# Performance work log

Hardware: AMD Instinct MI355X
Metric: run time of the kernel (lower is better)

## Reference

```python
import jax, jax.numpy as jnp
import numpy as np

B, T, D_IN, H, D = 4, 4096, 1024, 16, 64


def setup_inputs() -> dict:
    key = jax.random.key(0)
    k1, k2, k3 = jax.random.split(key, 3)
    inputs = jax.random.normal(k1, (B, T, D_IN), dtype=jnp.float32)
    kv_kernel = jax.random.normal(k2, (D_IN, H, D, 2), dtype=jnp.float32) * (1.0 / np.sqrt(D_IN))
    q_kernel = jax.random.normal(k3, (H, D), dtype=jnp.float32) * (1.0 / np.sqrt(D))
    return {"inputs": inputs, "kv_kernel": kv_kernel, "q_kernel": q_kernel}


def _associate(a, b):
    # Online-softmax combine on packed tuples [m(1), u(1), w(D)] along last axis.
    ma, ua, wa = a[..., :1], a[..., 1:2], a[..., 2:]
    mb, ub, wb = b[..., :1], b[..., 1:2], b[..., 2:]
    m = jnp.maximum(ma, mb)
    ea = jnp.exp(ma - m)
    eb = jnp.exp(mb - m)
    u = ua * ea + ub * eb
    w = wa * ea + wb * eb
    return jnp.concatenate([m, u, w], axis=-1)


def reference(inputs, kv_kernel, q_kernel):
    # inputs: (B,T,D_in); kv_kernel: (D_in,H,D,2); q_kernel: (H,D)
    kv = jnp.einsum('bti,ihdk->bthdk', inputs, kv_kernel)
    kv = jax.nn.relu(kv)  # activation; dropout disabled (inference)
    k = kv[..., 0]  # (B,T,H,D)
    v = kv[..., 1]  # (B,T,H,D)
    st = jnp.einsum('hd,bthd->bth', q_kernel, k)[..., None]  # (B,T,H,1)
    u_init = jnp.ones_like(st)  # exp(s - m) with m = s
    elems = jnp.concatenate([st, u_init, v], axis=-1)  # (B,T,H,D+2)
    o = jax.lax.associative_scan(_associate, elems, axis=1)
    c = o[..., 1:2]  # running denominator
    a = o[..., 2:]   # running numerator (B,T,H,D)
    h = a / c
    # concat_heads=False -> sum over heads
    return jnp.sum(h, axis=-2)  # (B,T,D)
```

## Files before the change

### kernel.cpp

```cpp
#include <hip/hip_runtime.h>
#include <hip/hip_bf16.h>
#include <math.h>

#define B_   4
#define T_   4096
#define DIN_ 1024
#define H_   16
#define D_   64
#define M_   (B_*T_)
#define N_   (H_*D_*2)
#define K_   DIN_
#define C_   64
#define CL_  (T_/C_)

typedef unsigned short u16;
typedef __attribute__((ext_vector_type(8))) short short8_t;
typedef __attribute__((ext_vector_type(4))) float float4_t;

__device__ __forceinline__ u16 f2bf(float f) {
  unsigned int x = __float_as_uint(f);
  x += 0x7fffu + ((x >> 16) & 1u);
  return (u16)(x >> 16);
}
__device__ __forceinline__ float bf2f(unsigned int u) {
  return __uint_as_float((u & 0xffffu) << 16);
}

__device__ __forceinline__ void g2l16(const u16* g, u16* l) {
  __builtin_amdgcn_global_load_lds(
      (const __attribute__((address_space(1))) void*)g,
      (__attribute__((address_space(3))) void*)l, 16, 0, 0);
}

__global__ __launch_bounds__(256)
void prep(const float* __restrict__ inputs, const float* __restrict__ kvk,
          u16* __restrict__ aB, u16* __restrict__ wBt) {
  __shared__ float tile[32][33];
  int bid = blockIdx.x;
  int tid = threadIdx.x;
  if (bid < 8192) {
    int i = bid * 256 + tid;
    const float4* src = (const float4*)inputs;
    float4 a = src[2*i], b = src[2*i+1];
    uint4 o;
    o.x = (unsigned)f2bf(a.x) | ((unsigned)f2bf(a.y) << 16);
    o.y = (unsigned)f2bf(a.z) | ((unsigned)f2bf(a.w) << 16);
    o.z = (unsigned)f2bf(b.x) | ((unsigned)f2bf(b.y) << 16);
    o.w = (unsigned)f2bf(b.z) | ((unsigned)f2bf(b.w) << 16);
    ((uint4*)aB)[i] = o;
  } else {
    int b2 = bid - 8192;
    int kb = (b2 & 31) * 32;
    int nb = (b2 >> 5) * 32;
    int r  = tid >> 3;
    int c4 = (tid & 7) * 4;
    float4 v = *(const float4*)&kvk[(size_t)(kb + r) * N_ + nb + c4];
    tile[r][c4+0] = v.x; tile[r][c4+1] = v.y; tile[r][c4+2] = v.z; tile[r][c4+3] = v.w;
    __syncthreads();
    unsigned lo = (unsigned)f2bf(tile[c4+0][r]) | ((unsigned)f2bf(tile[c4+1][r]) << 16);
    unsigned hi = (unsigned)f2bf(tile[c4+2][r]) | ((unsigned)f2bf(tile[c4+3][r]) << 16);
    uint2 o; o.x = lo; o.y = hi;
    *(uint2*)&wBt[(size_t)(nb + r) * K_ + kb + c4] = o;
  }
}

__global__ __launch_bounds__(256)
void gemm_kv(const u16* __restrict__ A, const u16* __restrict__ Bt,
             const float* __restrict__ q,
             float* __restrict__ sbuf, u16* __restrict__ vbuf) {
  __shared__ __align__(16) char smem[27136];
  u16*   lA    = (u16*)smem;
  u16*   lB    = (u16*)(smem + 8192);
  u16*   vtile = (u16*)smem;
  float* sred  = (float*)(smem + 18432);
  __shared__ float qs[D_];

  const int tid  = threadIdx.x;
  const int wave = tid >> 6;
  const int lane = tid & 63;
  const int quad = lane >> 4;
  const int l16  = lane & 15;
  const int h    = blockIdx.x;
  const int mt   = blockIdx.y;
  const int bm = mt * 128;
  const int bn = h * 128;
  const int wm = (wave >> 1) * 64;
  const int wn = (wave & 1) * 64;

  if (tid < D_) qs[tid] = q[h * D_ + tid];

  const int r4 = lane >> 2;
  const int cc = lane & 3;
  const int gk = ((cc ^ ((r4 >> 1) & 3))) * 8;
  const u16* ga0 = A  + (size_t)(bm + wave*16 + r4) * K_ + gk;
  const u16* ga1 = ga0 + (size_t)64 * K_;
  const u16* gb0 = Bt + (size_t)(bn + wave*16 + r4) * K_ + gk;
  const u16* gb1 = gb0 + (size_t)64 * K_;
  u16* la0 = lA + (wave*16) * 32;
  u16* la1 = lA + (64 + wave*16) * 32;
  u16* lb0 = lB + (wave*16) * 32;
  u16* lb1 = lB + (64 + wave*16) * 32;

  const int swz = (quad ^ ((l16 >> 1) & 3)) * 8;

  float4_t acc[4][4] = {};

  for (int k0 = 0; k0 < K_; k0 += 32) {
    __syncthreads();
    g2l16(ga0 + k0, la0);
    g2l16(ga1 + k0, la1);
    g2l16(gb0 + k0, lb0);
    g2l16(gb1 + k0, lb1);
    __syncthreads();

    short8_t af[4], bfr[4];
#pragma unroll
    for (int i = 0; i < 4; ++i)
      af[i] = *(const short8_t*)&lA[(wm + i*16 + l16) * 32 + swz];
#pragma unroll
    for (int j = 0; j < 4; ++j)
      bfr[j] = *(const short8_t*)&lB[(wn + j*16 + l16) * 32 + swz];
#pragma unroll
    for (int i = 0; i < 4; ++i)
#pragma unroll
      for (int j = 0; j < 4; ++j)
        acc[i][j] = __builtin_amdgcn_mfma_f32_16x16x32_bf16(af[i], bfr[j], acc[i][j], 0, 0, 0);
  }

  __syncthreads();

  if (l16 & 1) {
#pragma unroll
    for (int j = 0; j < 4; ++j) {
      int d = ((wn + j*16 + l16) & 127) >> 1;
#pragma unroll
      for (int i = 0; i < 4; ++i)
#pragma unroll
        for (int r = 0; r < 4; ++r) {
          int t = wm + i*16 + quad*4 + r;
          vtile[t*72 + d] = f2bf(fmaxf(acc[i][j][r], 0.f));
        }
    }
  } else {
    int slot = (wn >> 3) + (l16 >> 1);
#pragma unroll
    for (int i = 0; i < 4; ++i)
#pragma unroll
      for (int r = 0; r < 4; ++r) {
        int t = wm + i*16 + quad*4 + r;
        float p = 0.f;
#pragma unroll
        for (int j = 0; j < 4; ++j) {
          int d = ((wn + j*16 + l16) & 127) >> 1;
          p += qs[d] * fmaxf(acc[i][j][r], 0.f);
        }
        sred[t*17 + slot] = p;
      }
  }
  __syncthreads();

  const int b  = mt >> 5;
  const int t0 = (mt & 31) * 128;

  {
    int tr = tid >> 3;
    int d0 = (tid & 7) * 8;
    u16* vg = vbuf + ((size_t)(b * H_ + h) * T_ + t0) * D_;
#pragma unroll
    for (int it = 0; it < 4; ++it) {
      int t = tr + 32*it;
      uint4 val = *(const uint4*)&vtile[t*72 + d0];
      *(uint4*)&vg[(size_t)t * D_ + d0] = val;
    }
  }
  if (tid < 128) {
    float ssum = 0.f;
#pragma unroll
    for (int k = 0; k < 16; ++k) ssum += sred[tid*17 + k];
    sbuf[(size_t)(b * H_ + h) * T_ + t0 + tid] = ssum;
  }
}

__global__ __launch_bounds__(64)
void scan_pass1(const u16* __restrict__ vbuf, const float* __restrict__ sbuf,
                float* __restrict__ aggM, float* __restrict__ aggU,
                float* __restrict__ aggW) {
  __shared__ float sS[CL_];
  int blk = blockIdx.x;
  int bh  = blk >> 6;
  int c   = blk & (C_ - 1);
  int t0  = c * CL_;
  int tid = threadIdx.x;

  sS[tid] = sbuf[(size_t)bh * T_ + t0 + tid];
  __syncthreads();

  int d = tid;
  const u16* vp = vbuf + ((size_t)bh * T_ + t0) * D_ + d;
  float m = -INFINITY, u = 0.f, w = 0.f;
#pragma unroll 4
  for (int i = 0; i < CL_; ++i) {
    float si = sS[i];
    float v  = bf2f(vp[i * D_]);
    float mn    = fmaxf(m, si);
    float alpha = __expf(m - mn);
    float p     = __expf(si - mn);
    u = u * alpha + p;
    w = w * alpha + p * v;
    m = mn;
  }
  aggW[(size_t)blk * D_ + d] = w;
  if (d == 0) { aggM[blk] = m; aggU[blk] = u; }
}

__global__ __launch_bounds__(1024)
void scan_pass3(const u16* __restrict__ vbuf, const float* __restrict__ sbuf,
                const float* __restrict__ aggM, const float* __restrict__ aggU,
                const float* __restrict__ aggW, float* __restrict__ out) {
  __shared__ float sS[H_][CL_];
  __shared__ float wbuf[H_][8][D_ + 1];
  int bc = blockIdx.x;
  int b  = bc >> 6;
  int c  = bc & (C_ - 1);
  int tid  = threadIdx.x;
  int h    = tid >> 6;
  int lane = tid & 63;
  int bh   = b * H_ + h;
  int t0   = c * CL_;

  sS[h][lane] = sbuf[(size_t)bh * T_ + t0 + lane];

  float m = -INFINITY, u = 0.f, w = 0.f;
  for (int j = 0; j < c; ++j) {
    int idx = bh * C_ + j;
    float Mc = aggM[idx];
    float Uc = aggU[idx];
    float Wc = aggW[(size_t)idx * D_ + lane];
    float mn = fmaxf(m, Mc);
    float ea = __expf(m - mn);
    float eb = __expf(Mc - mn);
    u = u * ea + Uc * eb;
    w = w * ea + Wc * eb;
    m = mn;
  }
  __syncthreads();

  const u16* vp = vbuf + ((size_t)bh * T_ + t0) * D_ + lane;
  for (int g = 0; g < 8; ++g) {
#pragma unroll
    for (int ii = 0; ii < 8; ++ii) {
      int i = g * 8 + ii;
      float si = sS[h][i];
      float v  = bf2f(vp[i * D_]);
      float mn    = fmaxf(m, si);
      float alpha = __expf(m - mn);
      float p     = __expf(si - mn);
      u = u * alpha + p;
      w = w * alpha + p * v;
      m = mn;
      wbuf[h][ii][lane] = __fdividef(w, u);
    }
    __syncthreads();
    if (tid < 512) {
      int ii = tid >> 6, dd = tid & 63;
      float acc = 0.f;
#pragma unroll
      for (int hh = 0; hh < H_; ++hh) acc += wbuf[hh][ii][dd];
      out[((size_t)b * T_ + t0 + g*8 + ii) * D_ + dd] = acc;
    }
    __syncthreads();
  }
}

extern "C" void kernel_launch(void* const* d_in, const int* in_sizes, int n_in,
                              void* d_out, int out_size, void* d_ws, size_t ws_size,
                              hipStream_t stream) {
  const float* inputs = (const float*)d_in[0];
  const float* kvk    = (const float*)d_in[1];
  const float* qk     = (const float*)d_in[2];
  float* out = (float*)d_out;
  char* ws = (char*)d_ws;

  u16*   aB   = (u16*)ws;
  u16*   wBt  = (u16*)(ws + 33554432);
  u16*   vb   = (u16*)(ws + 37748736);
  float* sb   = (float*)(ws + 71303168);
  float* aggM = (float*)(ws + 72351744);
  float* aggU = (float*)(ws + 72368128);
  float* aggW = (float*)(ws + 72384512);

  prep<<<10240, 256, 0, stream>>>(inputs, kvk, aB, wBt);
  gemm_kv<<<dim3(H_, M_/128), 256, 0, stream>>>(aB, wBt, qk, sb, vb);
  scan_pass1<<<B_*H_*C_, 64, 0, stream>>>(vb, sb, aggM, aggU, aggW);
  scan_pass3<<<B_*C_, 1024, 0, stream>>>(vb, sb, aggM, aggU, aggW, out);
}
```

Baseline: 236.9 us.

## Fuse chunk scan into GEMM epilogue, double-buffer LDS, remap blocks per XCD

The per-chunk online-softmax reduction (the former scan_pass1) now runs inside the GEMM epilogue, reading V from LDS instead of re-reading vbuf from global memory, which removes one kernel launch. The GEMM main loop becomes double-buffered: the next K tile is issued before the current tile's MFMAs, leaving one barrier per iteration. The grid is flattened and remapped so that consecutive M tiles land on the same XCD, to improve L2 reuse. LDS use per block grows, and in the epilogue two waves run the serial scan while the other two write V out.

```diff
diff --git a/kernel.cpp b/kernel.cpp
--- a/kernel.cpp
+++ b/kernel.cpp
@@ -67,21 +67,26 @@
 __global__ __launch_bounds__(256)
 void gemm_kv(const u16* __restrict__ A, const u16* __restrict__ Bt,
              const float* __restrict__ q,
-             float* __restrict__ sbuf, u16* __restrict__ vbuf) {
-  __shared__ __align__(16) char smem[27136];
-  u16*   lA    = (u16*)smem;
-  u16*   lB    = (u16*)(smem + 8192);
+             float* __restrict__ sbuf, u16* __restrict__ vbuf,
+             float* __restrict__ aggM, float* __restrict__ aggU,
+             float* __restrict__ aggW) {
+  __shared__ __align__(16) char smem[33536];
   u16*   vtile = (u16*)smem;
   float* sred  = (float*)(smem + 18432);
-  __shared__ float qs[D_];
+  float* qs    = (float*)(smem + 32768);
+  float* sS    = (float*)(smem + 33024);
 
   const int tid  = threadIdx.x;
   const int wave = tid >> 6;
   const int lane = tid & 63;
   const int quad = lane >> 4;
   const int l16  = lane & 15;
-  const int h    = blockIdx.x;
-  const int mt   = blockIdx.y;
+
+  const int g    = blockIdx.x;
+  const int xcd  = g & 7;
+  const int slot = g >> 3;
+  const int h    = slot & 15;
+  const int mt   = (slot >> 4) * 8 + xcd;
   const int bm = mt * 128;
   const int bn = h * 128;
   const int wm = (wave >> 1) * 64;
@@ -96,30 +101,43 @@
   const u16* ga1 = ga0 + (size_t)64 * K_;
   const u16* gb0 = Bt + (size_t)(bn + wave*16 + r4) * K_ + gk;
   const u16* gb1 = gb0 + (size_t)64 * K_;
-  u16* la0 = lA + (wave*16) * 32;
-  u16* la1 = lA + (64 + wave*16) * 32;
-  u16* lb0 = lB + (wave*16) * 32;
-  u16* lb1 = lB + (64 + wave*16) * 32;
+  const int laOff = (wave*16) * 32;
+  const int lbOff = (wave*16) * 32;
 
   const int swz = (quad ^ ((l16 >> 1) & 3)) * 8;
 
   float4_t acc[4][4] = {};
 
-  for (int k0 = 0; k0 < K_; k0 += 32) {
+  {
+    u16* lA0 = (u16*)smem;
+    u16* lB0 = (u16*)(smem + 8192);
+    g2l16(ga0, lA0 + laOff);
+    g2l16(ga1, lA0 + laOff + 64*32);
+    g2l16(gb0, lB0 + lbOff);
+    g2l16(gb1, lB0 + lbOff + 64*32);
+  }
+
+  for (int it = 0; it < 32; ++it) {
+    u16* lAc = (u16*)(smem + (it & 1) * 16384);
+    u16* lBc = (u16*)(smem + (it & 1) * 16384 + 8192);
     __syncthreads();
-    g2l16(ga0 + k0, la0);
-    g2l16(ga1 + k0, la1);
-    g2l16(gb0 + k0, lb0);
-    g2l16(gb1 + k0, lb1);
-    __syncthreads();
+    if (it < 31) {
+      int kn = (it + 1) * 32;
+      u16* lAn = (u16*)(smem + ((it + 1) & 1) * 16384);
+      u16* lBn = (u16*)(smem + ((it + 1) & 1) * 16384 + 8192);
+      g2l16(ga0 + kn, lAn + laOff);
+      g2l16(ga1 + kn, lAn + laOff + 64*32);
+      g2l16(gb0 + kn, lBn + lbOff);
+      g2l16(gb1 + kn, lBn + lbOff + 64*32);
+    }
 
     short8_t af[4], bfr[4];
 #pragma unroll
     for (int i = 0; i < 4; ++i)
-      af[i] = *(const short8_t*)&lA[(wm + i*16 + l16) * 32 + swz];
+      af[i] = *(const short8_t*)&lAc[(wm + i*16 + l16) * 32 + swz];
 #pragma unroll
     for (int j = 0; j < 4; ++j)
-      bfr[j] = *(const short8_t*)&lB[(wn + j*16 + l16) * 32 + swz];
+      bfr[j] = *(const short8_t*)&lBc[(wn + j*16 + l16) * 32 + swz];
 #pragma unroll
     for (int i = 0; i < 4; ++i)
 #pragma unroll
@@ -142,7 +160,7 @@
         }
     }
   } else {
-    int slot = (wn >> 3) + (l16 >> 1);
+    int slot2 = (wn >> 3) + (l16 >> 1);
 #pragma unroll
     for (int i = 0; i < 4; ++i)
 #pragma unroll
@@ -154,63 +172,54 @@
           int d = ((wn + j*16 + l16) & 127) >> 1;
           p += qs[d] * fmaxf(acc[i][j][r], 0.f);
         }
-        sred[t*17 + slot] = p;
+        sred[t*17 + slot2] = p;
       }
   }
   __syncthreads();
 
-  const int b  = mt >> 5;
-  const int t0 = (mt & 31) * 128;
-
-  {
-    int tr = tid >> 3;
-    int d0 = (tid & 7) * 8;
-    u16* vg = vbuf + ((size_t)(b * H_ + h) * T_ + t0) * D_;
-#pragma unroll
-    for (int it = 0; it < 4; ++it) {
-      int t = tr + 32*it;
+  const int b   = mt >> 5;
+  const int tt0 = (mt & 31) * 128;
+  const int bh  = b * H_ + h;
+
+  if (tid < 128) {
+    float ssum = 0.f;
+#pragma unroll
+    for (int k = 0; k < 16; ++k) ssum += sred[tid*17 + k];
+    sS[tid] = ssum;
+    sbuf[(size_t)bh * T_ + tt0 + tid] = ssum;
+  }
+  __syncthreads();
+
+  if (wave < 2) {
+    int d = lane;
+    float m = -INFINITY, u = 0.f, w = 0.f;
+#pragma unroll 4
+    for (int i = 0; i < CL_; ++i) {
+      int t = wave * CL_ + i;
+      float si = sS[t];
+      float v  = bf2f(vtile[t*72 + d]);
+      float mn    = fmaxf(m, si);
+      float alpha = __expf(m - mn);
+      float p     = __expf(si - mn);
+      u = u * alpha + p;
+      w = w * alpha + p * v;
+      m = mn;
+    }
+    int blk = bh * C_ + (mt & 31) * 2 + wave;
+    aggW[(size_t)blk * D_ + d] = w;
+    if (d == 0) { aggM[blk] = m; aggU[blk] = u; }
+  } else {
+    int idx = tid - 128;
+    int d0  = (idx & 7) * 8;
+    int tr  = idx >> 3;
+    u16* vg = vbuf + ((size_t)bh * T_ + tt0) * D_;
+#pragma unroll
+    for (int itv = 0; itv < 8; ++itv) {
+      int t = tr + 16*itv;
       uint4 val = *(const uint4*)&vtile[t*72 + d0];
       *(uint4*)&vg[(size_t)t * D_ + d0] = val;
     }
   }
-  if (tid < 128) {
-    float ssum = 0.f;
-#pragma unroll
-    for (int k = 0; k < 16; ++k) ssum += sred[tid*17 + k];
-    sbuf[(size_t)(b * H_ + h) * T_ + t0 + tid] = ssum;
-  }
-}
-
-__global__ __launch_bounds__(64)
-void scan_pass1(const u16* __restrict__ vbuf, const float* __restrict__ sbuf,
-                float* __restrict__ aggM, float* __restrict__ aggU,
-                float* __restrict__ aggW) {
-  __shared__ float sS[CL_];
-  int blk = blockIdx.x;
-  int bh  = blk >> 6;
-  int c   = blk & (C_ - 1);
-  int t0  = c * CL_;
-  int tid = threadIdx.x;
-
-  sS[tid] = sbuf[(size_t)bh * T_ + t0 + tid];
-  __syncthreads();
-
-  int d = tid;
-  const u16* vp = vbuf + ((size_t)bh * T_ + t0) * D_ + d;
-  float m = -INFINITY, u = 0.f, w = 0.f;
-#pragma unroll 4
-  for (int i = 0; i < CL_; ++i) {
-    float si = sS[i];
-    float v  = bf2f(vp[i * D_]);
-    float mn    = fmaxf(m, si);
-    float alpha = __expf(m - mn);
-    float p     = __expf(si - mn);
-    u = u * alpha + p;
-    w = w * alpha + p * v;
-    m = mn;
-  }
-  aggW[(size_t)blk * D_ + d] = w;
-  if (d == 0) { aggM[blk] = m; aggU[blk] = u; }
 }
 
 __global__ __launch_bounds__(1024)
@@ -246,10 +255,10 @@
   __syncthreads();
 
   const u16* vp = vbuf + ((size_t)bh * T_ + t0) * D_ + lane;
-  for (int g = 0; g < 8; ++g) {
+  for (int gg = 0; gg < 8; ++gg) {
 #pragma unroll
     for (int ii = 0; ii < 8; ++ii) {
-      int i = g * 8 + ii;
+      int i = gg * 8 + ii;
       float si = sS[h][i];
       float v  = bf2f(vp[i * D_]);
       float mn    = fmaxf(m, si);
@@ -266,7 +275,7 @@
       float acc = 0.f;
 #pragma unroll
       for (int hh = 0; hh < H_; ++hh) acc += wbuf[hh][ii][dd];
-      out[((size_t)b * T_ + t0 + g*8 + ii) * D_ + dd] = acc;
+      out[((size_t)b * T_ + t0 + gg*8 + ii) * D_ + dd] = acc;
     }
     __syncthreads();
   }
@@ -290,7 +299,6 @@
   float* aggW = (float*)(ws + 72384512);
 
   prep<<<10240, 256, 0, stream>>>(inputs, kvk, aB, wBt);
-  gemm_kv<<<dim3(H_, M_/128), 256, 0, stream>>>(aB, wBt, qk, sb, vb);
-  scan_pass1<<<B_*H_*C_, 64, 0, stream>>>(vb, sb, aggM, aggU, aggW);
+  gemm_kv<<<2048, 256, 0, stream>>>(aB, wBt, qk, sb, vb, aggM, aggU, aggW);
   scan_pass3<<<B_*C_, 1024, 0, stream>>>(vb, sb, aggM, aggU, aggW, out);
 }
```

Result: no change. 239.7 us (+1.2%).
